# Performance work log

Hardware: AMD Instinct MI355X
Metric: run time of the kernel (lower is better)

## Reference

```python
import jax, jax.numpy as jnp
import numpy as np

H = 768
L = 9
M = 5            # max_span_length
CTX_RATIO = 0.5
NEG_INF = -1e30


def setup_inputs() -> dict:
    key = jax.random.key(0)
    ks = jax.random.split(key, 12)
    B, S = 4, 2048
    sc = 1.0 / np.sqrt(H)
    return {
        "sequence_output": jax.random.normal(ks[0], (B, S, H), dtype=jnp.float32),
        "Wc": jax.random.normal(ks[1], (H, L), dtype=jnp.float32) * sc,
        "bc": jnp.zeros((L,), dtype=jnp.float32),
        "wa": jax.random.normal(ks[2], (H,), dtype=jnp.float32) * sc,
        "ba": jnp.zeros((), dtype=jnp.float32),
        "W1": jax.random.normal(ks[3], (2 * H, H), dtype=jnp.float32) * (1.0 / np.sqrt(2 * H)),
        "b1": jnp.zeros((H,), dtype=jnp.float32),
        "gamma": jnp.ones((H,), dtype=jnp.float32),
        "beta": jnp.zeros((H,), dtype=jnp.float32),
        "W2": jax.random.normal(ks[4], (H, L), dtype=jnp.float32) * sc,
        "b2": jnp.zeros((L,), dtype=jnp.float32),
    }


def reference(sequence_output, Wc, bc, wa, ba, W1, b1, gamma, beta, W2, b2):
    x = sequence_output                        # [B,S,H]
    B, S, _ = x.shape
    base_logits = jnp.einsum('bsh,hl->bsl', x, Wc) + bc   # [B,S,L]

    # sliding-window indices: window [i-M, i+M] clipped to [0, S)
    offsets = jnp.arange(-M, M + 1)            # [W]
    idx = jnp.arange(S)[:, None] + offsets     # [S,W]
    valid = (idx >= 0) & (idx < S)             # [S,W]
    idx_c = jnp.clip(idx, 0, S - 1)            # [S,W]

    # attention scores over window (span_attention linear -> scalar per token)
    scores = jnp.einsum('bsh,h->bs', x, wa) + ba           # [B,S]
    win_scores = scores[:, idx_c]                          # [B,S,W]
    win_scores = jnp.where(valid[None], win_scores, NEG_INF)
    attn = jax.nn.softmax(win_scores, axis=-1)             # [B,S,W]

    win_tokens = x[:, idx_c]                               # [B,S,W,H] gather
    weighted_ctx = jnp.einsum('bsw,bswh->bsh', attn, win_tokens)

    token_with_ctx = jnp.concatenate([x, weighted_ctx], axis=-1)  # [B,S,2H]
    h = jnp.einsum('bsd,dh->bsh', token_with_ctx, W1) + b1
    # LayerNorm (eps = 1e-5, torch default)
    mu = jnp.mean(h, axis=-1, keepdims=True)
    var = jnp.mean((h - mu) ** 2, axis=-1, keepdims=True)
    h = (h - mu) * jax.lax.rsqrt(var + 1e-5) * gamma + beta
    h = jax.nn.gelu(h, approximate=False)                  # torch nn.GELU default (erf)
    ctx_logits = jnp.einsum('bsh,hl->bsl', h, W2) + b2

    return (1.0 - CTX_RATIO) * base_logits + CTX_RATIO * ctx_logits
```

## Files before the change

### kernel.cpp

```cpp
#include <hip/hip_runtime.h>
#include <hip/hip_bf16.h>
#include <math.h>

#define S_LEN 2048
#define BATCH 4
#define HDIM 768
#define LOUT 9
#define NROWS (BATCH*S_LEN)
#define K2H 1536
#define WIN 11
#define NEG_INF_F (-1e30f)

typedef __attribute__((ext_vector_type(4))) float f32x4;
typedef __attribute__((ext_vector_type(8))) short bf16x8;

static __device__ __forceinline__ void async_ld16(const void* g, void* l) {
  __builtin_amdgcn_global_load_lds((const __attribute__((address_space(1))) void*)g,
                                   (__attribute__((address_space(3))) void*)l, 16, 0, 0);
}

static __device__ __forceinline__ unsigned short f2bf(float f) {
  union { float f; unsigned int u; } v; v.f = f;
  unsigned int u = v.u;
  unsigned int r = (u + 0x7fffu + ((u >> 16) & 1u)) >> 16;
  return (unsigned short)r;
}

__global__ __launch_bounds__(256) void k_prep_w1t(const float* __restrict__ W1,
                                                  unsigned short* __restrict__ W1t) {
  __shared__ float tile[32][33];
  int bk = blockIdx.x % 48;
  int bn = blockIdx.x / 48;
  int tc = threadIdx.x % 32;
  int tr = threadIdx.x / 32;
  #pragma unroll
  for (int i = 0; i < 32; i += 8) {
    tile[tr + i][tc] = W1[(bk*32 + tr + i) * HDIM + bn*32 + tc];
  }
  __syncthreads();
  #pragma unroll
  for (int i = 0; i < 32; i += 8) {
    W1t[(bn*32 + tr + i) * K2H + bk*32 + tc] = f2bf(tile[tc][tr + i]);
  }
}

__global__ __launch_bounds__(256) void k_ctx(const float* __restrict__ x,
                                             const float* __restrict__ wa,
                                             const float* __restrict__ ba,
                                             const float* __restrict__ Wc,
                                             const float* __restrict__ bc,
                                             unsigned short* __restrict__ xc,
                                             float* __restrict__ base) {
  __shared__ float sred[4][WIN];
  __shared__ float redp[4][LOUT];
  int row = blockIdx.x;
  int b = row >> 11, s = row & 2047;
  int t = threadIdx.x;
  int lane = t & 63, wave = t >> 6;

  float xv[WIN][3];
  bool vld[WIN];
  #pragma unroll
  for (int w = 0; w < WIN; ++w) {
    int j = s - 5 + w;
    bool valid = (j >= 0) && (j < S_LEN);
    vld[w] = valid;
    int jc = valid ? j : (j < 0 ? 0 : S_LEN - 1);
    const float* xr = x + (b * S_LEN + jc) * HDIM;
    xv[w][0] = xr[t];
    xv[w][1] = xr[t + 256];
    xv[w][2] = xr[t + 512];
  }
  float wa0 = wa[t], wa1 = wa[t + 256], wa2 = wa[t + 512];

  float sp[WIN];
  #pragma unroll
  for (int w = 0; w < WIN; ++w)
    sp[w] = xv[w][0] * wa0 + xv[w][1] * wa1 + xv[w][2] * wa2;
  #pragma unroll
  for (int w = 0; w < WIN; ++w)
    #pragma unroll
    for (int m = 1; m < 64; m <<= 1) sp[w] += __shfl_xor(sp[w], m);
  if (lane == 0) {
    #pragma unroll
    for (int w = 0; w < WIN; ++w) sred[wave][w] = sp[w];
  }
  __syncthreads();
  float bav = ba[0];
  float sc[WIN];
  #pragma unroll
  for (int w = 0; w < WIN; ++w) {
    float v = sred[0][w] + sred[1][w] + sred[2][w] + sred[3][w] + bav;
    sc[w] = vld[w] ? v : NEG_INF_F;
  }
  float mx = sc[0];
  #pragma unroll
  for (int w = 1; w < WIN; ++w) mx = fmaxf(mx, sc[w]);
  float es[WIN], ssum = 0.f;
  #pragma unroll
  for (int w = 0; w < WIN; ++w) {
    es[w] = vld[w] ? __expf(sc[w] - mx) : 0.f;
    ssum += es[w];
  }
  float inv = 1.f / ssum;

  float c0 = 0.f, c1 = 0.f, c2 = 0.f;
  #pragma unroll
  for (int w = 0; w < WIN; ++w) {
    float aw = es[w] * inv;
    c0 += aw * xv[w][0];
    c1 += aw * xv[w][1];
    c2 += aw * xv[w][2];
  }
  unsigned short* dstc = xc + row * K2H;
  dstc[t]       = f2bf(xv[5][0]);
  dstc[t + 256] = f2bf(xv[5][1]);
  dstc[t + 512] = f2bf(xv[5][2]);
  dstc[HDIM + t]       = f2bf(c0);
  dstc[HDIM + t + 256] = f2bf(c1);
  dstc[HDIM + t + 512] = f2bf(c2);

  float p[LOUT] = {};
  #pragma unroll
  for (int i = 0; i < 3; ++i) {
    int e = t + i * 256;
    float xvv = xv[5][i];
    const float* wrow = Wc + e * LOUT;
    #pragma unroll
    for (int l = 0; l < LOUT; ++l) p[l] += xvv * wrow[l];
  }
  #pragma unroll
  for (int l = 0; l < LOUT; ++l)
    #pragma unroll
    for (int m = 1; m < 64; m <<= 1) p[l] += __shfl_xor(p[l], m);
  if (lane == 0) {
    #pragma unroll
    for (int l = 0; l < LOUT; ++l) redp[wave][l] = p[l];
  }
  __syncthreads();
  if (t < LOUT) {
    base[row * LOUT + t] = redp[0][t] + redp[1][t] + redp[2][t] + redp[3][t] + bc[t];
  }
}

__global__ __launch_bounds__(256, 4) void k_gemm(const unsigned short* __restrict__ A,
                                                 const unsigned short* __restrict__ Bt,
                                                 const float* __restrict__ b1,
                                                 float* __restrict__ Hout) {
  __shared__ unsigned short As[2][128 * 32];
  __shared__ unsigned short Bs[2][64 * 32];
  int bid = blockIdx.x;
  int obid = (bid & 7) * 96 + (bid >> 3);
  int bm = obid / 12, bn = obid % 12;
  int t = threadIdx.x;
  int lane = t & 63, wave = t >> 6;

  int fl = ((lane >> 2) ^ (lane >> 4)) & 3;
  int sSrc = ((lane & 3) ^ fl);
  int rIn = lane >> 2;

  const unsigned short* gA = A  + (bm * 128 + wave * 32 + rIn) * K2H + sSrc * 8;
  const unsigned short* gB = Bt + (bn * 64  + wave * 16 + rIn) * K2H + sSrc * 8;

  f32x4 acc[2][4] = {};

  int laneRow = lane & 15;
  int slot = lane >> 4;
  int fr = ((lane & 3) ^ ((lane >> 2) & 3));
  int rdOff = ((slot ^ fr) & 3) * 8;

#define STAGE(buf, kt) do {                                                    \
    async_ld16(gA + (kt),             &As[buf][(wave * 32) * 32]);             \
    async_ld16(gA + 16 * K2H + (kt),  &As[buf][(wave * 32 + 16) * 32]);        \
    async_ld16(gB + (kt),             &Bs[buf][(wave * 16) * 32]);             \
  } while (0)

#define COMPUTE(buf) do {                                                      \
    bf16x8 af[2], bfv[4];                                                      \
    _Pragma("unroll")                                                          \
    for (int m = 0; m < 2; ++m)                                                \
      af[m] = *(const bf16x8*)(&As[buf][(wave * 32 + m * 16 + laneRow) * 32 + rdOff]); \
    _Pragma("unroll")                                                          \
    for (int n = 0; n < 4; ++n)                                                \
      bfv[n] = *(const bf16x8*)(&Bs[buf][(n * 16 + laneRow) * 32 + rdOff]);    \
    _Pragma("unroll")                                                          \
    for (int m = 0; m < 2; ++m)                                                \
      _Pragma("unroll")                                                        \
      for (int n = 0; n < 4; ++n)                                              \
        acc[m][n] = __builtin_amdgcn_mfma_f32_16x16x32_bf16(af[m], bfv[n], acc[m][n], 0, 0, 0); \
  } while (0)

  STAGE(0, 0);
  __syncthreads();
  int cur = 0;
  for (int kt = 32; kt < K2H; kt += 32) {
    STAGE(cur ^ 1, kt);
    COMPUTE(cur);
    __syncthreads();
    cur ^= 1;
  }
  COMPUTE(cur);

  int orow = bm * 128 + wave * 32 + (lane >> 4) * 4;
  int ocol = bn * 64 + (lane & 15);
  #pragma unroll
  for (int m = 0; m < 2; ++m)
    #pragma unroll
    for (int n = 0; n < 4; ++n) {
      int col = ocol + n * 16;
      float bv = b1[col];
      #pragma unroll
      for (int r = 0; r < 4; ++r) {
        Hout[(orow + m * 16 + r) * HDIM + col] = acc[m][n][r] + bv;
      }
    }
#undef STAGE
#undef COMPUTE
}

__global__ __launch_bounds__(256) void k_ln(const float* __restrict__ Hin,
                                            const float* __restrict__ gamma,
                                            const float* __restrict__ beta,
                                            const float* __restrict__ W2,
                                            const float* __restrict__ b2,
                                            const float* __restrict__ base,
                                            float* __restrict__ out) {
  __shared__ float redS[4], redQ[4], redp[4][LOUT];
  int row = blockIdx.x;
  int t = threadIdx.x;
  int lane = t & 63, wave = t >> 6;
  const float* hr = Hin + row * HDIM;
  float v0 = hr[t], v1 = hr[t + 256], v2 = hr[t + 512];
  float s1 = v0 + v1 + v2;
  float s2 = v0 * v0 + v1 * v1 + v2 * v2;
  #pragma unroll
  for (int m = 1; m < 64; m <<= 1) { s1 += __shfl_xor(s1, m); s2 += __shfl_xor(s2, m); }
  if (lane == 0) { redS[wave] = s1; redQ[wave] = s2; }
  __syncthreads();
  s1 = redS[0] + redS[1] + redS[2] + redS[3];
  s2 = redQ[0] + redQ[1] + redQ[2] + redQ[3];
  float mu = s1 * (1.f / HDIM);
  float var = s2 * (1.f / HDIM) - mu * mu;
  float rstd = rsqrtf(var + 1e-5f);
  float p[LOUT] = {};
  float vv[3] = { v0, v1, v2 };
  #pragma unroll
  for (int i = 0; i < 3; ++i) {
    int e = t + i * 256;
    float g = (vv[i] - mu) * rstd * gamma[e] + beta[e];
    float gg = 0.5f * g * (1.f + erff(g * 0.70710678118654752f));
    const float* wrow = W2 + e * LOUT;
    #pragma unroll
    for (int l = 0; l < LOUT; ++l) p[l] += gg * wrow[l];
  }
  #pragma unroll
  for (int l = 0; l < LOUT; ++l)
    #pragma unroll
    for (int m = 1; m < 64; m <<= 1) p[l] += __shfl_xor(p[l], m);
  if (lane == 0) {
    #pragma unroll
    for (int l = 0; l < LOUT; ++l) redp[wave][l] = p[l];
  }
  __syncthreads();
  if (t < LOUT) {
    float cl = redp[0][t] + redp[1][t] + redp[2][t] + redp[3][t] + b2[t];
    out[row * LOUT + t] = 0.5f * base[row * LOUT + t] + 0.5f * cl;
  }
}

extern "C" void kernel_launch(void* const* d_in, const int* in_sizes, int n_in,
                              void* d_out, int out_size, void* d_ws, size_t ws_size,
                              hipStream_t stream) {
  const float* x     = (const float*)d_in[0];
  const float* Wc    = (const float*)d_in[1];
  const float* bc    = (const float*)d_in[2];
  const float* wa    = (const float*)d_in[3];
  const float* ba    = (const float*)d_in[4];
  const float* W1    = (const float*)d_in[5];
  const float* b1    = (const float*)d_in[6];
  const float* gamma = (const float*)d_in[7];
  const float* beta  = (const float*)d_in[8];
  const float* W2    = (const float*)d_in[9];
  const float* b2    = (const float*)d_in[10];
  float* out = (float*)d_out;

  char* ws = (char*)d_ws;
  unsigned short* xc  = (unsigned short*)(ws);
  unsigned short* w1t = (unsigned short*)(ws + 25165824);
  float* base         = (float*)(ws + 27525120);
  float* hbuf         = (float*)(ws + 27820032);

  k_prep_w1t<<<dim3(1152), dim3(256), 0, stream>>>(W1, w1t);
  k_ctx     <<<dim3(8192), dim3(256), 0, stream>>>(x, wa, ba, Wc, bc, xc, base);
  k_gemm    <<<dim3(768),  dim3(256), 0, stream>>>(xc, w1t, b1, hbuf);
  k_ln      <<<dim3(8192), dim3(256), 0, stream>>>(hbuf, gamma, beta, W2, b2, base, out);
}
```

Measured before the change: 205.3 us.

## Split context kernel into score/prep pass and windowed bf16 context pass

The fused context kernel, which loaded all 11 window rows of fp32 x per token and recomputed each neighbour's attention score, is split into two kernels. The first writes the bf16 copy of x, each row's attention score and the base logits. The second reads the 11 precomputed scores and gathers neighbour rows from the bf16 buffer. This removes the 11x redundant score dot-products and halves the bytes read per gathered row, at the cost of an extra launch and a bf16-rounded context input.

```diff
diff --git a/kernel.cpp b/kernel.cpp
--- a/kernel.cpp
+++ b/kernel.cpp
@@ -26,6 +26,11 @@
   return (unsigned short)r;
 }
 
+static __device__ __forceinline__ float bf2f(unsigned short h) {
+  union { unsigned int u; float f; } v; v.u = ((unsigned int)h) << 16;
+  return v.f;
+}
+
 __global__ __launch_bounds__(256) void k_prep_w1t(const float* __restrict__ W1,
                                                   unsigned short* __restrict__ W1t) {
   __shared__ float tile[32][33];
@@ -44,103 +49,92 @@
   }
 }
 
-__global__ __launch_bounds__(256) void k_ctx(const float* __restrict__ x,
-                                             const float* __restrict__ wa,
-                                             const float* __restrict__ ba,
-                                             const float* __restrict__ Wc,
-                                             const float* __restrict__ bc,
-                                             unsigned short* __restrict__ xc,
-                                             float* __restrict__ base) {
-  __shared__ float sred[4][WIN];
-  __shared__ float redp[4][LOUT];
-  int row = blockIdx.x;
+__global__ __launch_bounds__(192) void k_prep(const float* __restrict__ x,
+                                              const float* __restrict__ wa,
+                                              const float* __restrict__ ba,
+                                              const float* __restrict__ Wc,
+                                              const float* __restrict__ bc,
+                                              unsigned short* __restrict__ xc,
+                                              float* __restrict__ scores,
+                                              float* __restrict__ base) {
+  __shared__ float red[3][LOUT + 1];
+  int bid = blockIdx.x;
+  int row = (bid & 7) * 1024 + (bid >> 3);
+  int t = threadIdx.x;
+  int lane = t & 63, wave = t >> 6;
+  const float4 v = *(const float4*)(x + row * HDIM + t * 4);
+  const float4 w = *(const float4*)(wa + t * 4);
+  ushort4 o;
+  o.x = f2bf(v.x); o.y = f2bf(v.y); o.z = f2bf(v.z); o.w = f2bf(v.w);
+  *(ushort4*)(xc + row * K2H + t * 4) = o;
+
+  float pv[LOUT + 1];
+  pv[LOUT] = v.x * w.x + v.y * w.y + v.z * w.z + v.w * w.w;
+  #pragma unroll
+  for (int l = 0; l < LOUT; ++l) pv[l] = 0.f;
+  const float xvv[4] = { v.x, v.y, v.z, v.w };
+  #pragma unroll
+  for (int j = 0; j < 4; ++j) {
+    const float* wr = Wc + (t * 4 + j) * LOUT;
+    #pragma unroll
+    for (int l = 0; l < LOUT; ++l) pv[l] += xvv[j] * wr[l];
+  }
+  #pragma unroll
+  for (int l = 0; l <= LOUT; ++l)
+    #pragma unroll
+    for (int m = 1; m < 64; m <<= 1) pv[l] += __shfl_xor(pv[l], m);
+  if (lane == 0) {
+    #pragma unroll
+    for (int l = 0; l <= LOUT; ++l) red[wave][l] = pv[l];
+  }
+  __syncthreads();
+  if (t < LOUT) {
+    base[row * LOUT + t] = red[0][t] + red[1][t] + red[2][t] + bc[t];
+  } else if (t == LOUT) {
+    scores[row] = red[0][LOUT] + red[1][LOUT] + red[2][LOUT] + ba[0];
+  }
+}
+
+__global__ __launch_bounds__(192) void k_ctx(const float* __restrict__ scores,
+                                             unsigned short* __restrict__ xc) {
+  __shared__ float swin[WIN];
+  int bid = blockIdx.x;
+  int row = (bid & 7) * 1024 + (bid >> 3);
   int b = row >> 11, s = row & 2047;
   int t = threadIdx.x;
-  int lane = t & 63, wave = t >> 6;
-
-  float xv[WIN][3];
-  bool vld[WIN];
+  if (t < WIN) {
+    int j = s - 5 + t;
+    bool valid = (j >= 0) && (j < S_LEN);
+    int jc = valid ? j : (j < 0 ? 0 : S_LEN - 1);
+    swin[t] = valid ? scores[b * S_LEN + jc] : NEG_INF_F;
+  }
+  __syncthreads();
+  float mx = swin[0];
+  #pragma unroll
+  for (int w = 1; w < WIN; ++w) mx = fmaxf(mx, swin[w]);
+  float es[WIN], ssum = 0.f;
   #pragma unroll
   for (int w = 0; w < WIN; ++w) {
-    int j = s - 5 + w;
-    bool valid = (j >= 0) && (j < S_LEN);
-    vld[w] = valid;
-    int jc = valid ? j : (j < 0 ? 0 : S_LEN - 1);
-    const float* xr = x + (b * S_LEN + jc) * HDIM;
-    xv[w][0] = xr[t];
-    xv[w][1] = xr[t + 256];
-    xv[w][2] = xr[t + 512];
-  }
-  float wa0 = wa[t], wa1 = wa[t + 256], wa2 = wa[t + 512];
-
-  float sp[WIN];
-  #pragma unroll
-  for (int w = 0; w < WIN; ++w)
-    sp[w] = xv[w][0] * wa0 + xv[w][1] * wa1 + xv[w][2] * wa2;
-  #pragma unroll
-  for (int w = 0; w < WIN; ++w)
-    #pragma unroll
-    for (int m = 1; m < 64; m <<= 1) sp[w] += __shfl_xor(sp[w], m);
-  if (lane == 0) {
-    #pragma unroll
-    for (int w = 0; w < WIN; ++w) sred[wave][w] = sp[w];
-  }
-  __syncthreads();
-  float bav = ba[0];
-  float sc[WIN];
-  #pragma unroll
-  for (int w = 0; w < WIN; ++w) {
-    float v = sred[0][w] + sred[1][w] + sred[2][w] + sred[3][w] + bav;
-    sc[w] = vld[w] ? v : NEG_INF_F;
-  }
-  float mx = sc[0];
-  #pragma unroll
-  for (int w = 1; w < WIN; ++w) mx = fmaxf(mx, sc[w]);
-  float es[WIN], ssum = 0.f;
-  #pragma unroll
-  for (int w = 0; w < WIN; ++w) {
-    es[w] = vld[w] ? __expf(sc[w] - mx) : 0.f;
+    float sv = swin[w];
+    es[w] = (sv > -1e29f) ? __expf(sv - mx) : 0.f;
     ssum += es[w];
   }
   float inv = 1.f / ssum;
-
-  float c0 = 0.f, c1 = 0.f, c2 = 0.f;
+  float c0 = 0.f, c1 = 0.f, c2 = 0.f, c3 = 0.f;
   #pragma unroll
   for (int w = 0; w < WIN; ++w) {
     float aw = es[w] * inv;
-    c0 += aw * xv[w][0];
-    c1 += aw * xv[w][1];
-    c2 += aw * xv[w][2];
-  }
-  unsigned short* dstc = xc + row * K2H;
-  dstc[t]       = f2bf(xv[5][0]);
-  dstc[t + 256] = f2bf(xv[5][1]);
-  dstc[t + 512] = f2bf(xv[5][2]);
-  dstc[HDIM + t]       = f2bf(c0);
-  dstc[HDIM + t + 256] = f2bf(c1);
-  dstc[HDIM + t + 512] = f2bf(c2);
-
-  float p[LOUT] = {};
-  #pragma unroll
-  for (int i = 0; i < 3; ++i) {
-    int e = t + i * 256;
-    float xvv = xv[5][i];
-    const float* wrow = Wc + e * LOUT;
-    #pragma unroll
-    for (int l = 0; l < LOUT; ++l) p[l] += xvv * wrow[l];
-  }
-  #pragma unroll
-  for (int l = 0; l < LOUT; ++l)
-    #pragma unroll
-    for (int m = 1; m < 64; m <<= 1) p[l] += __shfl_xor(p[l], m);
-  if (lane == 0) {
-    #pragma unroll
-    for (int l = 0; l < LOUT; ++l) redp[wave][l] = p[l];
-  }
-  __syncthreads();
-  if (t < LOUT) {
-    base[row * LOUT + t] = redp[0][t] + redp[1][t] + redp[2][t] + redp[3][t] + bc[t];
-  }
+    int j = s - 5 + w;
+    int jc = (j < 0) ? 0 : ((j >= S_LEN) ? S_LEN - 1 : j);
+    const ushort4 uv = *(const ushort4*)(xc + (((long)b * S_LEN + jc) * K2H) + t * 4);
+    c0 += aw * bf2f(uv.x);
+    c1 += aw * bf2f(uv.y);
+    c2 += aw * bf2f(uv.z);
+    c3 += aw * bf2f(uv.w);
+  }
+  ushort4 o;
+  o.x = f2bf(c0); o.y = f2bf(c1); o.z = f2bf(c2); o.w = f2bf(c3);
+  *(ushort4*)(xc + row * K2H + HDIM + t * 4) = o;
 }
 
 __global__ __launch_bounds__(256, 4) void k_gemm(const unsigned short* __restrict__ A,
@@ -287,11 +281,13 @@
   char* ws = (char*)d_ws;
   unsigned short* xc  = (unsigned short*)(ws);
   unsigned short* w1t = (unsigned short*)(ws + 25165824);
-  float* base         = (float*)(ws + 27525120);
-  float* hbuf         = (float*)(ws + 27820032);
+  float* scores       = (float*)(ws + 27525120);
+  float* base         = (float*)(ws + 27557888);
+  float* hbuf         = (float*)(ws + 27852800);
 
   k_prep_w1t<<<dim3(1152), dim3(256), 0, stream>>>(W1, w1t);
-  k_ctx     <<<dim3(8192), dim3(256), 0, stream>>>(x, wa, ba, Wc, bc, xc, base);
+  k_prep    <<<dim3(8192), dim3(192), 0, stream>>>(x, wa, ba, Wc, bc, xc, scores, base);
+  k_ctx     <<<dim3(8192), dim3(192), 0, stream>>>(scores, xc);
   k_gemm    <<<dim3(768),  dim3(256), 0, stream>>>(xc, w1t, b1, hbuf);
   k_ln      <<<dim3(8192), dim3(256), 0, stream>>>(hbuf, gamma, beta, W2, b2, base, out);
 }
```

New measurement: 183.5 us. 10.6% less time.
